# Kernel tuning notes

Hardware: AMD Instinct MI355X
Metric: run time of the kernel (lower is better)

Reference implementation:

```python
import jax, jax.numpy as jnp
import numpy as np

M0, M1 = 16, 16          # n_modes
C = 64                   # hidden_channels
B = 16                   # batch
H = W = 128              # spatial resolution
SCALE = C ** (-2)        # matches torch: scale * torch.rand(...)


def setup_inputs() -> dict:
    key = jax.random.key(0)
    kx, k0r, k0i, k1r, k1i = jax.random.split(key, 5)
    X = jax.random.normal(kx, (B, C, H, W), dtype=jnp.float32)
    wshape = (C, C, M0, M1)
    # torch.rand with cfloat draws U[0,1) for real and imag parts independently
    w0r = SCALE * jax.random.uniform(k0r, wshape, dtype=jnp.float32)
    w0i = SCALE * jax.random.uniform(k0i, wshape, dtype=jnp.float32)
    w1r = SCALE * jax.random.uniform(k1r, wshape, dtype=jnp.float32)
    w1i = SCALE * jax.random.uniform(k1i, wshape, dtype=jnp.float32)
    return {"X": X, "w0r": w0r, "w0i": w0i, "w1r": w1r, "w1i": w1i}


def reference(X, w0r, w0i, w1r, w1i):
    w0 = w0r + 1j * w0i                       # linear0: (C, C, M0, M1) complex
    w1 = w1r + 1j * w1i                       # linear1
    Xf = jnp.fft.rfftn(X, axes=(-2, -1), norm="forward")   # (B, C, H, W//2+1) complex
    # out[b,c] = sum_t weight[c,t] * Xf[b,t] on the two kept-mode corners
    top = jnp.einsum("ctxy,btxy->bcxy", w0, Xf[:, :, :M0, :M1])
    bot = jnp.einsum("ctxy,btxy->bcxy", w1, Xf[:, :, -M0:, :M1])
    Y = jnp.zeros_like(Xf)
    Y = Y.at[:, :, :M0, :M1].set(top)
    Y = Y.at[:, :, -M0:, :M1].set(bot)
    out = jnp.fft.irfftn(Y, axes=(-2, -1), s=(H, W), norm="forward")
    return out.astype(jnp.float32)
```

## Files before the change

kernel.cpp:

```cpp
#include <hip/hip_runtime.h>

#define PI2 6.28318530717958647692f

__global__ __launch_bounds__(256) void k_fwd(const float* __restrict__ X,
                                             float* __restrict__ Xf) {
  __shared__ __attribute__((aligned(16))) float E1t[64 * 32 * 2];
  __shared__ __attribute__((aligned(16))) float A2t[128 * 33 * 2];
  const int plane = blockIdx.x;
  const int tid = threadIdx.x;
  const float* Xp = X + (size_t)plane * (128 * 128);

  #pragma unroll
  for (int k = 0; k < 8; ++k) {
    int idx = tid + k * 256;
    int h = idx >> 5, kxi = idx & 31;
    int kx = kxi + ((kxi & 16) ? 96 : 0);
    float s_, c_;
    __sincosf(-PI2 * (float)((kx * h) & 127) * (1.f / 128.f), &s_, &c_);
    E1t[idx * 2] = c_; E1t[idx * 2 + 1] = s_;
  }
  __syncthreads();

  {
    const int w2 = tid & 63;
    const int kxg = tid >> 6;
    float cr[8][2], ci[8][2];
    #pragma unroll
    for (int j = 0; j < 8; ++j) {
      cr[j][0] = cr[j][1] = 0.f; ci[j][0] = ci[j][1] = 0.f;
    }
    float2 xa = *(const float2*)&Xp[w2 * 2];
    float2 xb = *(const float2*)&Xp[64 * 128 + w2 * 2];
    for (int h = 0; h < 64; ++h) {
      float2 na = make_float2(0.f, 0.f), nb = make_float2(0.f, 0.f);
      if (h < 63) {
        na = *(const float2*)&Xp[(h + 1) * 128 + w2 * 2];
        nb = *(const float2*)&Xp[(h + 65) * 128 + w2 * 2];
      }
      float ue0 = xa.x + xb.x, ue1 = xa.y + xb.y;
      float uo0 = xa.x - xb.x, uo1 = xa.y - xb.y;
      const float4* Er = (const float4*)&E1t[(h * 32 + kxg * 8) * 2];
      #pragma unroll
      for (int j2 = 0; j2 < 4; ++j2) {
        float4 e = Er[j2];
        int je = 2 * j2, jo = 2 * j2 + 1;
        cr[je][0] = fmaf(ue0, e.x, cr[je][0]);
        ci[je][0] = fmaf(ue0, e.y, ci[je][0]);
        cr[je][1] = fmaf(ue1, e.x, cr[je][1]);
        ci[je][1] = fmaf(ue1, e.y, ci[je][1]);
        cr[jo][0] = fmaf(uo0, e.z, cr[jo][0]);
        ci[jo][0] = fmaf(uo0, e.w, ci[jo][0]);
        cr[jo][1] = fmaf(uo1, e.z, cr[jo][1]);
        ci[jo][1] = fmaf(uo1, e.w, ci[jo][1]);
      }
      xa = na; xb = nb;
    }
    #pragma unroll
    for (int u = 0; u < 2; ++u) {
      int w = 2 * w2 + u;
      #pragma unroll
      for (int j = 0; j < 8; ++j) {
        int f2i = w * 33 + 8 * kxg + j;
        A2t[f2i * 2] = cr[j][u]; A2t[f2i * 2 + 1] = ci[j][u];
      }
    }
  }
  __syncthreads();

  {
    const int kxi = tid >> 3;
    const int t = tid & 7;
    const float s = (t & 1) ? -1.f : 1.f;
    float d0r, d0i, d1r, d1i;
    __sincosf(-PI2 * (float)t * (1.f / 128.f), &d0i, &d0r);
    __sincosf(-PI2 * (float)(t + 8) * (1.f / 128.f), &d1i, &d1r);
    float T0r = 1.f, T0i = 0.f, T1r = 1.f, T1i = 0.f;
    float r0 = 0.f, i0 = 0.f, r1 = 0.f, i1 = 0.f;
    #pragma unroll 4
    for (int w = 0; w < 64; ++w) {
      const float2 a = *(const float2*)&A2t[(w * 33 + kxi) * 2];
      const float2 b = *(const float2*)&A2t[((w + 64) * 33 + kxi) * 2];
      float ur = fmaf(s, b.x, a.x);
      float ui = fmaf(s, b.y, a.y);
      r0 = fmaf(ur, T0r, r0); r0 = fmaf(-ui, T0i, r0);
      i0 = fmaf(ur, T0i, i0); i0 = fmaf(ui, T0r, i0);
      r1 = fmaf(ur, T1r, r1); r1 = fmaf(-ui, T1i, r1);
      i1 = fmaf(ur, T1i, i1); i1 = fmaf(ui, T1r, i1);
      float n0r = T0r * d0r - T0i * d0i, n0i = T0r * d0i + T0i * d0r;
      float n1r = T1r * d1r - T1i * d1i, n1i = T1r * d1i + T1i * d1r;
      T0r = n0r; T0i = n0i; T1r = n1r; T1i = n1i;
    }
    const float sc = 1.f / 16384.f;
    float* base = Xf + (size_t)plane * 1024 + kxi * 32;
    *(float2*)&base[t * 2]       = make_float2(r0 * sc, i0 * sc);
    *(float2*)&base[(t + 8) * 2] = make_float2(r1 * sc, i1 * sc);
  }
}

__global__ __launch_bounds__(256) void k_mix(const float* __restrict__ Xf,
                                             const float* __restrict__ w0r,
                                             const float* __restrict__ w0i,
                                             const float* __restrict__ w1r,
                                             const float* __restrict__ w1i,
                                             float* __restrict__ Y) {
  __shared__ __attribute__((aligned(16))) float Wl[4 * 64 * 16 * 2];
  const int bid = blockIdx.x;
  const int c2 = bid >> 8;
  const int x  = (bid >> 4) & 15;
  const int cg = bid & 15;
  const int c0 = cg * 4;
  const int kxi = c2 * 16 + x;
  const float* Wr_g = c2 ? w1r : w0r;
  const float* Wi_g = c2 ? w1i : w0i;
  const int tid = threadIdx.x;
  const int b = tid >> 4;
  const int y = tid & 15;

  #pragma unroll
  for (int k = 0; k < 16; ++k) {
    int idx = tid + k * 256;
    int y_ = idx & 15, t_ = (idx >> 4) & 63, c_ = idx >> 10;
    size_t ga = (((size_t)(c0 + c_) * 64 + t_) * 16 + x) * 16 + y_;
    float wr = Wr_g[ga], wi = Wi_g[ga];
    Wl[idx * 2] = wr; Wl[idx * 2 + 1] = wi;
  }
  __syncthreads();

  float aR[4] = {}, aI[4] = {};
  const float* xbase = Xf + ((size_t)b * 64) * 1024 + kxi * 32 + y * 2;
  for (int t8 = 0; t8 < 64; t8 += 8) {
    float2 xv[8];
    #pragma unroll
    for (int q = 0; q < 8; ++q)
      xv[q] = *(const float2*)&xbase[(size_t)(t8 + q) * 1024];
    #pragma unroll
    for (int q = 0; q < 8; ++q) {
      int t = t8 + q;
      #pragma unroll
      for (int cj = 0; cj < 4; ++cj) {
        const float2 wv = *(const float2*)&Wl[((cj * 64 + t) * 16 + y) * 2];
        aR[cj] = fmaf(xv[q].x, wv.x, aR[cj]);
        aR[cj] = fmaf(-xv[q].y, wv.y, aR[cj]);
        aI[cj] = fmaf(xv[q].x, wv.y, aI[cj]);
        aI[cj] = fmaf(xv[q].y, wv.x, aI[cj]);
      }
    }
  }
  #pragma unroll
  for (int cj = 0; cj < 4; ++cj) {
    size_t ya = ((size_t)(b * 64 + c0 + cj)) * 1024 + kxi * 32 + y * 2;
    *(float2*)&Y[ya] = make_float2(aR[cj], aI[cj]);
  }
}

__global__ __launch_bounds__(256) void k_inv(const float* __restrict__ Y,
                                             float* __restrict__ out) {
  __shared__ __attribute__((aligned(16))) float Yl[1024];
  __shared__ __attribute__((aligned(16))) float Ml[128 * 18 * 2];
  const int plane = blockIdx.x;
  const int tid = threadIdx.x;
  {
    *(float4*)&Yl[tid * 4] = *(const float4*)&Y[(size_t)plane * 1024 + tid * 4];
  }
  __syncthreads();

  {
    const int g = tid >> 7;
    const int h = tid & 127;
    float zr[8] = {}, zi[8] = {};
    float uw, uwi;
    __sincosf(PI2 * (float)h * (1.f / 128.f), &uwi, &uw);
    const float4* Yl4 = (const float4*)Yl;
    float Tr = 1.f, Ti = 0.f;
    #pragma unroll 4
    for (int kxi = 0; kxi < 16; ++kxi) {
      #pragma unroll
      for (int q = 0; q < 4; ++q) {
        float4 p = Yl4[kxi * 8 + g * 4 + q];
        int m = 2 * q;
        zr[m]   = fmaf(p.x, Tr, zr[m]);   zr[m]   = fmaf(-p.y, Ti, zr[m]);
        zi[m]   = fmaf(p.x, Ti, zi[m]);   zi[m]   = fmaf(p.y, Tr, zi[m]);
        zr[m+1] = fmaf(p.z, Tr, zr[m+1]); zr[m+1] = fmaf(-p.w, Ti, zr[m+1]);
        zi[m+1] = fmaf(p.z, Ti, zi[m+1]); zi[m+1] = fmaf(p.w, Tr, zi[m+1]);
      }
      float nr = Tr * uw - Ti * uwi, ni = Tr * uwi + Ti * uw;
      Tr = nr; Ti = ni;
    }
    __sincosf(PI2 * (float)((112 * h) & 127) * (1.f / 128.f), &Ti, &Tr);
    #pragma unroll 4
    for (int kxi = 16; kxi < 32; ++kxi) {
      #pragma unroll
      for (int q = 0; q < 4; ++q) {
        float4 p = Yl4[kxi * 8 + g * 4 + q];
        int m = 2 * q;
        zr[m]   = fmaf(p.x, Tr, zr[m]);   zr[m]   = fmaf(-p.y, Ti, zr[m]);
        zi[m]   = fmaf(p.x, Ti, zi[m]);   zi[m]   = fmaf(p.y, Tr, zi[m]);
        zr[m+1] = fmaf(p.z, Tr, zr[m+1]); zr[m+1] = fmaf(-p.w, Ti, zr[m+1]);
        zi[m+1] = fmaf(p.z, Ti, zi[m+1]); zi[m+1] = fmaf(p.w, Tr, zi[m+1]);
      }
      float nr = Tr * uw - Ti * uwi, ni = Tr * uwi + Ti * uw;
      Tr = nr; Ti = ni;
    }
    #pragma unroll
    for (int m = 0; m < 8; ++m) {
      int ky = g * 8 + m;
      float f = (ky == 0) ? 1.f : 2.f;
      int f2i = h * 18 + ky;
      Ml[f2i * 2]     =  f * zr[m];
      Ml[f2i * 2 + 1] = -f * zi[m];
    }
  }
  __syncthreads();

  {
    const int hq = tid >> 6;
    const int w = tid & 63;
    float C[16], S[16];
    {
      float cw, sw;
      __sincosf(PI2 * (float)w * (1.f / 128.f), &sw, &cw);
      C[0] = 1.f; S[0] = 0.f;
      #pragma unroll
      for (int k = 1; k < 16; ++k) {
        C[k] = C[k - 1] * cw - S[k - 1] * sw;
        S[k] = C[k - 1] * sw + S[k - 1] * cw;
      }
    }
    float* op = out + (size_t)plane * (128 * 128);
    const float4* Ml4 = (const float4*)Ml;
    #pragma unroll 2
    for (int hj = 0; hj < 32; ++hj) {
      int h = hq * 32 + hj;
      float e = 0.f, o = 0.f;
      #pragma unroll
      for (int j2 = 0; j2 < 8; ++j2) {
        float4 m01 = Ml4[h * 9 + j2];
        int k = 2 * j2;
        float t0 = m01.x * C[k] + m01.y * S[k];
        float t1 = m01.z * C[k + 1] + m01.w * S[k + 1];
        e += t0; o += t1;
      }
      op[h * 128 + w]      = e + o;
      op[h * 128 + w + 64] = e - o;
    }
  }
}

extern "C" void kernel_launch(void* const* d_in, const int* in_sizes, int n_in,
                              void* d_out, int out_size, void* d_ws, size_t ws_size,
                              hipStream_t stream) {
  const float* X   = (const float*)d_in[0];
  const float* w0r = (const float*)d_in[1];
  const float* w0i = (const float*)d_in[2];
  const float* w1r = (const float*)d_in[3];
  const float* w1i = (const float*)d_in[4];
  float* outp = (float*)d_out;
  float* Xf = (float*)d_ws;
  float* Yw = (float*)d_ws + (1u << 20);
  k_fwd<<<1024, 256, 0, stream>>>(X, Xf);
  k_mix<<<512, 256, 0, stream>>>(Xf, w0r, w0i, w1r, w1i, Yw);
  k_inv<<<1024, 256, 0, stream>>>(Yw, outp);
}
```

Baseline: 184.3 us.

## Replace twiddle table with recurrence in forward FFT and stage Xf tiles in mix

The forward kernel drops the shared-memory twiddle table. Each thread now handles two kx rows over eight w columns, reads X with wider float4 loads, and steps twiddles by complex recurrence, re-seeding them exactly at h=32. The intermediate layout is transposed to kx-major with padding, so stores are float4 and the second stage reads change to match. The mix kernel now stages Xf chunks in shared memory with coalesced float4 loads instead of strided per-thread float2 global loads. The costs are more synchronisation and a small loss of accuracy from the recurrence.

```diff
diff --git a/kernel.cpp b/kernel.cpp
--- a/kernel.cpp
+++ b/kernel.cpp
@@ -4,65 +4,66 @@
 
 __global__ __launch_bounds__(256) void k_fwd(const float* __restrict__ X,
                                              float* __restrict__ Xf) {
-  __shared__ __attribute__((aligned(16))) float E1t[64 * 32 * 2];
-  __shared__ __attribute__((aligned(16))) float A2t[128 * 33 * 2];
+  __shared__ __attribute__((aligned(16))) float A2t[32 * 130 * 2];
   const int plane = blockIdx.x;
   const int tid = threadIdx.x;
   const float* Xp = X + (size_t)plane * (128 * 128);
 
-  #pragma unroll
-  for (int k = 0; k < 8; ++k) {
-    int idx = tid + k * 256;
-    int h = idx >> 5, kxi = idx & 31;
-    int kx = kxi + ((kxi & 16) ? 96 : 0);
-    float s_, c_;
-    __sincosf(-PI2 * (float)((kx * h) & 127) * (1.f / 128.f), &s_, &c_);
-    E1t[idx * 2] = c_; E1t[idx * 2 + 1] = s_;
-  }
-  __syncthreads();
-
-  {
-    const int w2 = tid & 63;
-    const int kxg = tid >> 6;
-    float cr[8][2], ci[8][2];
-    #pragma unroll
-    for (int j = 0; j < 8; ++j) {
-      cr[j][0] = cr[j][1] = 0.f; ci[j][0] = ci[j][1] = 0.f;
-    }
-    float2 xa = *(const float2*)&Xp[w2 * 2];
-    float2 xb = *(const float2*)&Xp[64 * 128 + w2 * 2];
+  {
+    const int kp = tid >> 4;
+    const int wq = tid & 15;
+    const int w0 = wq * 8;
+    const int kie = 2 * kp;
+    const int kxe = kie + ((kie & 16) ? 96 : 0);
+    const int kxo = kxe + 1;
+    float der, dei, dor_, doi;
+    __sincosf(-PI2 * (float)kxe * (1.f / 128.f), &dei, &der);
+    __sincosf(-PI2 * (float)kxo * (1.f / 128.f), &doi, &dor_);
+    float aer[8], aei[8], aor[8], aoi[8];
+    #pragma unroll
+    for (int j = 0; j < 8; ++j) { aer[j] = aei[j] = aor[j] = aoi[j] = 0.f; }
+
+    float4 xa0 = *(const float4*)&Xp[w0];
+    float4 xa1 = *(const float4*)&Xp[w0 + 4];
+    float4 xb0 = *(const float4*)&Xp[64 * 128 + w0];
+    float4 xb1 = *(const float4*)&Xp[64 * 128 + w0 + 4];
+    float Ter = 1.f, Tei = 0.f, Tor = 1.f, Toi = 0.f;
+
     for (int h = 0; h < 64; ++h) {
-      float2 na = make_float2(0.f, 0.f), nb = make_float2(0.f, 0.f);
+      float4 na0 = make_float4(0, 0, 0, 0), na1 = na0, nb0 = na0, nb1 = na0;
       if (h < 63) {
-        na = *(const float2*)&Xp[(h + 1) * 128 + w2 * 2];
-        nb = *(const float2*)&Xp[(h + 65) * 128 + w2 * 2];
-      }
-      float ue0 = xa.x + xb.x, ue1 = xa.y + xb.y;
-      float uo0 = xa.x - xb.x, uo1 = xa.y - xb.y;
-      const float4* Er = (const float4*)&E1t[(h * 32 + kxg * 8) * 2];
-      #pragma unroll
-      for (int j2 = 0; j2 < 4; ++j2) {
-        float4 e = Er[j2];
-        int je = 2 * j2, jo = 2 * j2 + 1;
-        cr[je][0] = fmaf(ue0, e.x, cr[je][0]);
-        ci[je][0] = fmaf(ue0, e.y, ci[je][0]);
-        cr[je][1] = fmaf(ue1, e.x, cr[je][1]);
-        ci[je][1] = fmaf(ue1, e.y, ci[je][1]);
-        cr[jo][0] = fmaf(uo0, e.z, cr[jo][0]);
-        ci[jo][0] = fmaf(uo0, e.w, ci[jo][0]);
-        cr[jo][1] = fmaf(uo1, e.z, cr[jo][1]);
-        ci[jo][1] = fmaf(uo1, e.w, ci[jo][1]);
-      }
-      xa = na; xb = nb;
-    }
-    #pragma unroll
-    for (int u = 0; u < 2; ++u) {
-      int w = 2 * w2 + u;
+        na0 = *(const float4*)&Xp[(h + 1) * 128 + w0];
+        na1 = *(const float4*)&Xp[(h + 1) * 128 + w0 + 4];
+        nb0 = *(const float4*)&Xp[(h + 65) * 128 + w0];
+        nb1 = *(const float4*)&Xp[(h + 65) * 128 + w0 + 4];
+      }
+      if (h == 32) {
+        __sincosf(-PI2 * (float)((kxe * 32) & 127) * (1.f / 128.f), &Tei, &Ter);
+        __sincosf(-PI2 * (float)((kxo * 32) & 127) * (1.f / 128.f), &Toi, &Tor);
+      }
+      float xa[8] = {xa0.x, xa0.y, xa0.z, xa0.w, xa1.x, xa1.y, xa1.z, xa1.w};
+      float xb[8] = {xb0.x, xb0.y, xb0.z, xb0.w, xb1.x, xb1.y, xb1.z, xb1.w};
       #pragma unroll
       for (int j = 0; j < 8; ++j) {
-        int f2i = w * 33 + 8 * kxg + j;
-        A2t[f2i * 2] = cr[j][u]; A2t[f2i * 2 + 1] = ci[j][u];
-      }
+        float ue = xa[j] + xb[j];
+        float uo = xa[j] - xb[j];
+        aer[j] = fmaf(ue, Ter, aer[j]);
+        aei[j] = fmaf(ue, Tei, aei[j]);
+        aor[j] = fmaf(uo, Tor, aor[j]);
+        aoi[j] = fmaf(uo, Toi, aoi[j]);
+      }
+      float ner = Ter * der - Tei * dei, nei = Ter * dei + Tei * der;
+      float nor_ = Tor * dor_ - Toi * doi, noi = Tor * doi + Toi * dor_;
+      Ter = ner; Tei = nei; Tor = nor_; Toi = noi;
+      xa0 = na0; xa1 = na1; xb0 = nb0; xb1 = nb1;
+    }
+    #pragma unroll
+    for (int j2 = 0; j2 < 4; ++j2) {
+      int j = 2 * j2;
+      *(float4*)&A2t[(kie * 130 + w0 + j) * 2] =
+          make_float4(aer[j], aei[j], aer[j + 1], aei[j + 1]);
+      *(float4*)&A2t[((kie + 1) * 130 + w0 + j) * 2] =
+          make_float4(aor[j], aoi[j], aor[j + 1], aoi[j + 1]);
     }
   }
   __syncthreads();
@@ -78,8 +79,8 @@
     float r0 = 0.f, i0 = 0.f, r1 = 0.f, i1 = 0.f;
     #pragma unroll 4
     for (int w = 0; w < 64; ++w) {
-      const float2 a = *(const float2*)&A2t[(w * 33 + kxi) * 2];
-      const float2 b = *(const float2*)&A2t[((w + 64) * 33 + kxi) * 2];
+      const float2 a = *(const float2*)&A2t[(kxi * 130 + w) * 2];
+      const float2 b = *(const float2*)&A2t[(kxi * 130 + w + 64) * 2];
       float ur = fmaf(s, b.x, a.x);
       float ui = fmaf(s, b.y, a.y);
       r0 = fmaf(ur, T0r, r0); r0 = fmaf(-ui, T0i, r0);
@@ -104,6 +105,7 @@
                                              const float* __restrict__ w1i,
                                              float* __restrict__ Y) {
   __shared__ __attribute__((aligned(16))) float Wl[4 * 64 * 16 * 2];
+  __shared__ __attribute__((aligned(16))) float Xs[16 * 16 * 18 * 2];
   const int bid = blockIdx.x;
   const int c2 = bid >> 8;
   const int x  = (bid >> 4) & 15;
@@ -124,25 +126,31 @@
     float wr = Wr_g[ga], wi = Wi_g[ga];
     Wl[idx * 2] = wr; Wl[idx * 2 + 1] = wi;
   }
-  __syncthreads();
 
   float aR[4] = {}, aI[4] = {};
-  const float* xbase = Xf + ((size_t)b * 64) * 1024 + kxi * 32 + y * 2;
-  for (int t8 = 0; t8 < 64; t8 += 8) {
-    float2 xv[8];
-    #pragma unroll
-    for (int q = 0; q < 8; ++q)
-      xv[q] = *(const float2*)&xbase[(size_t)(t8 + q) * 1024];
-    #pragma unroll
-    for (int q = 0; q < 8; ++q) {
-      int t = t8 + q;
+  for (int tc = 0; tc < 4; ++tc) {
+    __syncthreads();
+    #pragma unroll
+    for (int k = 0; k < 8; ++k) {
+      int idx = tid + k * 256;
+      int q = idx & 7, tb = idx >> 3;
+      int t_ = tb >> 4, b_ = tb & 15;
+      const float4 v = *(const float4*)&Xf[(size_t)(b_ * 64 + tc * 16 + t_) * 1024 +
+                                           kxi * 32 + q * 4];
+      *(float4*)&Xs[((t_ * 16 + b_) * 18 + 2 * q) * 2] = v;
+    }
+    __syncthreads();
+    #pragma unroll
+    for (int t = 0; t < 16; ++t) {
+      const float2 xv = *(const float2*)&Xs[((t * 16 + b) * 18 + y) * 2];
+      const int tt = tc * 16 + t;
       #pragma unroll
       for (int cj = 0; cj < 4; ++cj) {
-        const float2 wv = *(const float2*)&Wl[((cj * 64 + t) * 16 + y) * 2];
-        aR[cj] = fmaf(xv[q].x, wv.x, aR[cj]);
-        aR[cj] = fmaf(-xv[q].y, wv.y, aR[cj]);
-        aI[cj] = fmaf(xv[q].x, wv.y, aI[cj]);
-        aI[cj] = fmaf(xv[q].y, wv.x, aI[cj]);
+        const float2 wv = *(const float2*)&Wl[((cj * 64 + tt) * 16 + y) * 2];
+        aR[cj] = fmaf(xv.x, wv.x, aR[cj]);
+        aR[cj] = fmaf(-xv.y, wv.y, aR[cj]);
+        aI[cj] = fmaf(xv.x, wv.y, aI[cj]);
+        aI[cj] = fmaf(xv.y, wv.x, aI[cj]);
       }
     }
   }
```

After: 198.4 us. +7.6%, slower.
